# Kernel optimization log

Measured on AMD Instinct MI355X. Metric: run time of the kernel, lower is better.

Reference implementation:

```python
import jax, jax.numpy as jnp
import numpy as np

NUM_ENT = 10000
NUM_REL = 230
S_DIM = 96
T_DIM = 32
DIM = S_DIM + T_DIM  # 128
N = 32768   # neighbors
Q = 4096    # unique query entities
E = 32768   # pooling edges
B = 1024    # batch triples
BN_EPS = 1e-5


def setup_inputs() -> dict:
    key = jax.random.key(0)
    ks = jax.random.split(key, 32)
    inp = {}
    inp["neighbor_idx"] = jax.random.randint(ks[0], (N,), 0, NUM_ENT)
    inp["rel_id"] = jax.random.randint(ks[1], (N,), 0, 2 * NUM_REL)
    inp["years"] = jax.random.uniform(ks[2], (N, 1), jnp.float32)
    inp["months"] = jax.random.uniform(ks[3], (N, 1), jnp.float32)
    inp["days"] = jax.random.uniform(ks[4], (N, 1), jnp.float32)
    inp["pool_src"] = jax.random.randint(ks[5], (E,), 0, N)
    inp["pool_dst"] = jax.random.randint(ks[6], (E,), 0, Q)
    inp["head_pos"] = jax.random.randint(ks[7], (B,), 0, Q)
    inp["tail_pos"] = jax.random.randint(ks[8], (B,), 0, Q)
    inp["rels"] = jax.random.randint(ks[9], (B,), 0, NUM_REL)
    # parameters (xavier-ish scales)
    inp["ent_embs"] = jax.random.normal(ks[10], (NUM_ENT, S_DIM), jnp.float32) * 0.05
    names = ["y_freq", "y_phi", "y_amp", "m_freq", "m_phi", "m_amp", "d_freq", "d_phi", "d_amp"]
    for i, n in enumerate(names):
        inp[n] = jax.random.normal(ks[11 + i], (NUM_ENT, T_DIM), jnp.float32) * 0.05
    inp["rel_embs"] = jax.random.normal(ks[20], (NUM_REL, DIM), jnp.float32) * 0.05
    inp["W"] = jax.random.normal(ks[21], (2 * NUM_REL, DIM, DIM), jnp.float32) * (1.0 / np.sqrt(DIM))
    inp["b"] = jnp.zeros((2 * NUM_REL, DIM), jnp.float32)
    inp["gamma"] = jnp.ones((2 * NUM_REL, DIM), jnp.float32)
    inp["beta"] = jnp.zeros((2 * NUM_REL, DIM), jnp.float32)
    return inp


def _forward(ent_embs, y_freq, y_phi, y_amp, m_freq, m_phi, m_amp,
             d_freq, d_phi, d_amp, rel_embs, W, b, gamma, beta,
             years, months, days,
             neighbor_idx, rel_id, pool_src, pool_dst, head_pos, tail_pos, rels):
    # diachronic time embedding: amp * sin(freq * t + phi), summed over y/m/d
    ty = y_amp[neighbor_idx] * jnp.sin(y_freq[neighbor_idx] * years + y_phi[neighbor_idx])
    tm = m_amp[neighbor_idx] * jnp.sin(m_freq[neighbor_idx] * months + m_phi[neighbor_idx])
    td = d_amp[neighbor_idx] * jnp.sin(d_freq[neighbor_idx] * days + d_phi[neighbor_idx])
    x = jnp.concatenate([ent_embs[neighbor_idx], ty + tm + td], axis=1)  # [N, DIM]

    # per-relation Linear (gather weights per neighbor)
    z = jnp.einsum('nd,nde->ne', x, W[rel_id]) + b[rel_id]  # [N, DIM]

    # per-relation-bucket BatchNorm (training stats, biased var); skipped for singleton buckets
    R2 = 2 * NUM_REL
    cnt = jax.ops.segment_sum(jnp.ones((z.shape[0],), z.dtype), rel_id, num_segments=R2)
    denom = jnp.maximum(cnt, 1.0)[:, None]
    mean = jax.ops.segment_sum(z, rel_id, num_segments=R2) / denom
    var = jax.ops.segment_sum(z * z, rel_id, num_segments=R2) / denom - mean * mean
    var = jnp.maximum(var, 0.0)
    zn = (z - mean[rel_id]) * jax.lax.rsqrt(var[rel_id] + BN_EPS) * gamma[rel_id] + beta[rel_id]
    z = jnp.where((cnt[rel_id] > 1.0)[:, None], zn, z)
    z = jax.nn.relu(z)

    # average pooling of neighbor features per query entity (PoolingLayer 'avg')
    psum = jax.ops.segment_sum(z[pool_src], pool_dst, num_segments=Q)
    pcnt = jax.ops.segment_sum(jnp.ones((pool_src.shape[0],), z.dtype), pool_dst, num_segments=Q)
    emb = psum / jnp.maximum(pcnt, 1.0)[:, None]  # [Q, DIM]

    # TransE-style scoring: -||h + r - t||_2 (dropout p=0 / eval mode)
    diff = emb[head_pos] + rel_embs[rels] - emb[tail_pos]
    return -jnp.sqrt(jnp.sum(diff * diff, axis=1))


def reference(neighbor_idx, rel_id, years, months, days, pool_src, pool_dst,
              head_pos, tail_pos, rels, ent_embs, y_freq, y_phi, y_amp,
              m_freq, m_phi, m_amp, d_freq, d_phi, d_amp, rel_embs, W, b, gamma, beta):
    return _forward(ent_embs, y_freq, y_phi, y_amp, m_freq, m_phi, m_amp,
                    d_freq, d_phi, d_amp, rel_embs, W, b, gamma, beta,
                    years, months, days,
                    neighbor_idx, rel_id, pool_src, pool_dst, head_pos, tail_pos, rels)
```

## Files before the change

### kernel.cpp

```cpp
#include <hip/hip_runtime.h>
#include <math.h>

#define NUM_ENT 10000
#define NUM_REL 230
#define R2      460
#define S_DIM   96
#define T_DIM   32
#define DIM     128
#define N_NBR   32768
#define Q_ENT   4096
#define E_EDGE  32768
#define B_TRI   1024
#define BN_EPS  1e-5f
#define CHUNK   64

typedef __attribute__((ext_vector_type(8))) short bf16x8;
typedef __attribute__((ext_vector_type(4))) float f32x4;

__device__ __forceinline__ unsigned short f2bf(float f) {
    unsigned int u = __float_as_uint(f);
    u = (u + 0x7FFFu + ((u >> 16) & 1u)) >> 16;
    return (unsigned short)u;
}
__device__ __forceinline__ float bf2f(unsigned short us) {
    return __uint_as_float((unsigned int)us << 16);
}

__device__ __forceinline__ int XIDX(int m, int d) {
    return (m * DIM + d) ^ ((m & 7) << 3);
}

__global__ void k_zero(int* __restrict__ p, int n4) {
    int i = blockIdx.x * blockDim.x + threadIdx.x;
    if (i < n4) ((int4*)p)[i] = make_int4(0, 0, 0, 0);
}

__global__ __launch_bounds__(256, 2) void k_front(
    const float* __restrict__ W, unsigned short* __restrict__ Wfrag,
    const int* __restrict__ rel, const int* __restrict__ psrc,
    const int* __restrict__ pdst,
    int* __restrict__ hist_rel, int* __restrict__ histE,
    int* __restrict__ pcnt,
    int* __restrict__ ticket_n, int* __restrict__ ticket_e)
{
    const int t = threadIdx.x;
    if (blockIdx.x >= R2) {
        const int i = (blockIdx.x - R2) * 256 + t;
        if (i < N_NBR) ticket_n[i] = atomicAdd(&hist_rel[rel[i]], 1);
        if (i < E_EDGE) {
            const int s = psrc[i];
            ticket_e[i] = atomicAdd(&histE[rel[s]], 1);
            atomicAdd(&pcnt[pdst[i]], 1);
        }
        return;
    }
    const int r = blockIdx.x;
    __shared__ float Wl[DIM * DIM];
    {
        const float4* Wg = (const float4*)(W + (size_t)r * DIM * DIM);
        float4* Wl4 = (float4*)Wl;
        #pragma unroll
        for (int i = 0; i < 16; ++i)
            Wl4[t + i * 256] = Wg[t + i * 256];
    }
    __syncthreads();
    unsigned short* dst = Wfrag + (size_t)r * DIM * DIM;
    #pragma unroll
    for (int it = 0; it < 8; ++it) {
        const int id = t + it * 256;
        const int lane = id & 63;
        const int h    = (id >> 6) & 1;
        const int wv   = (id >> 7) & 3;
        const int kk   = (id >> 9) & 3;
        const int n  = 32 * wv + 16 * h + (lane & 15);
        const int kb = 32 * kk + 8 * (lane >> 4);
        ushort4 lo, hi;
        lo.x = f2bf(Wl[(kb + 0) * DIM + n]);
        lo.y = f2bf(Wl[(kb + 1) * DIM + n]);
        lo.z = f2bf(Wl[(kb + 2) * DIM + n]);
        lo.w = f2bf(Wl[(kb + 3) * DIM + n]);
        hi.x = f2bf(Wl[(kb + 4) * DIM + n]);
        hi.y = f2bf(Wl[(kb + 5) * DIM + n]);
        hi.z = f2bf(Wl[(kb + 6) * DIM + n]);
        hi.w = f2bf(Wl[(kb + 7) * DIM + n]);
        *(ushort4*)&dst[id * 8]     = lo;
        *(ushort4*)&dst[id * 8 + 4] = hi;
    }
}

__global__ __launch_bounds__(256) void k_place(
    const int* __restrict__ rel, const int* __restrict__ psrc,
    const int* __restrict__ pdst,
    const int* __restrict__ hist_rel, const int* __restrict__ histE,
    const int* __restrict__ ticket_n, const int* __restrict__ ticket_e,
    int* __restrict__ offsets, int* __restrict__ eoff,
    int* __restrict__ order, int* __restrict__ rankpack,
    int* __restrict__ epack)
{
    __shared__ int hA[512], hB[512], part[256];
    const int t = threadIdx.x;
    const int b = blockIdx.x;
    hA[t]       = (t < R2) ? hist_rel[t] : 0;
    hA[t + 256] = (t + 256 < R2) ? hist_rel[t + 256] : 0;
    hB[t]       = (t < R2) ? histE[t] : 0;
    hB[t + 256] = (t + 256 < R2) ? histE[t + 256] : 0;
    __syncthreads();

    const int a0 = hA[2 * t], a1 = hA[2 * t + 1];
    part[t] = a0 + a1;
    __syncthreads();
    for (int off = 1; off < 256; off <<= 1) {
        int v = (t >= off) ? part[t - off] : 0;
        __syncthreads();
        part[t] += v;
        __syncthreads();
    }
    {
        const int ex = t ? part[t - 1] : 0;
        hA[2 * t] = ex; hA[2 * t + 1] = ex + a0;
        if (b == 0) {
            if (2 * t < R2)     offsets[2 * t]     = ex;
            if (2 * t + 1 < R2) offsets[2 * t + 1] = ex + a0;
            if (t == 255)       offsets[R2]        = part[255];
        }
    }
    __syncthreads();

    const int b0 = hB[2 * t], b1 = hB[2 * t + 1];
    part[t] = b0 + b1;
    __syncthreads();
    for (int off = 1; off < 256; off <<= 1) {
        int v = (t >= off) ? part[t - off] : 0;
        __syncthreads();
        part[t] += v;
        __syncthreads();
    }
    {
        const int ex = t ? part[t - 1] : 0;
        hB[2 * t] = ex; hB[2 * t + 1] = ex + b0;
        if (b == 0) {
            if (2 * t < R2)     eoff[2 * t]     = ex;
            if (2 * t + 1 < R2) eoff[2 * t + 1] = ex + b0;
            if (t == 255)       eoff[R2]        = part[255];
        }
    }
    __syncthreads();

    const int i = b * 256 + t;
    if (i < N_NBR) {
        const int r = rel[i];
        const int pos = hA[r] + ticket_n[i];
        order[pos] = i;
        rankpack[i] = pos;
    }
    if (i < E_EDGE) {
        const int s = psrc[i];
        const int kr = rel[s];
        const int epos = hB[kr] + ticket_e[i];
        epack[epos] = s | (pdst[i] << 15);
    }
}

__global__ __launch_bounds__(512, 4) void k_matvec(
    const int* __restrict__ order, const int* __restrict__ offsets,
    const int* __restrict__ eoff, const int* __restrict__ epack,
    const int* __restrict__ rankpack,
    const int* __restrict__ nbr,
    const float* __restrict__ years, const float* __restrict__ months, const float* __restrict__ days,
    const float* __restrict__ ent,
    const float* __restrict__ yf, const float* __restrict__ yp, const float* __restrict__ ya,
    const float* __restrict__ mf, const float* __restrict__ mp, const float* __restrict__ ma,
    const float* __restrict__ df, const float* __restrict__ dp, const float* __restrict__ da,
    const unsigned short* __restrict__ Wfrag, const float* __restrict__ bias,
    const float* __restrict__ gamma, const float* __restrict__ beta,
    unsigned short* __restrict__ z_s, float* __restrict__ psum)
{
    const int r     = blockIdx.x;
    const int start = offsets[r];
    const int cnt   = offsets[r + 1] - start;

    __shared__ __align__(16) unsigned short Xl[2][CHUNK * DIM];
    __shared__ int s_ord[2][CHUNK];
    __shared__ int s_ni[2][CHUNK];
    __shared__ float bnred[8][2][16][2];
    __shared__ float scl[DIM], shf[DIM];

    const int t    = threadIdx.x;
    const int wid  = t >> 6;
    const int half = wid >> 2;
    const int wv   = wid & 3;
    const int lane = t & 63;
    const int l15  = lane & 15;
    const int g    = lane >> 4;

    const int nn0 = 32 * wv + l15;
    const int nn1 = nn0 + 16;
    const float bv0 = bias[r * DIM + nn0];
    const float bv1 = bias[r * DIM + nn1];

    float lsum0 = 0.f, lsq0 = 0.f, lsum1 = 0.f, lsq1 = 0.f;
    const unsigned short* Wr = Wfrag + (size_t)r * DIM * DIM;

    for (int cbase = 0; cbase < cnt; cbase += 2 * CHUNK) {
        const int hbase = cbase + half * CHUNK;
        const int mcnt  = min(CHUNK, max(0, cnt - hbase));

        if (t < 2 * CHUNK) {
            const int hh = t >> 6;
            const int m  = t & 63;
            const int gb = cbase + hh * CHUNK;
            int o = -1, ni = 0;
            if (gb + m < cnt) { o = order[start + gb + m]; ni = nbr[o]; }
            s_ord[hh][m] = o;
            s_ni[hh][m]  = ni;
        }
        __syncthreads();

        if (mcnt > 0) {
            const int lt = t & 255;
            const int m = lt >> 2, s = lt & 3;
            const int ni = s_ni[half][m];
            const bool vm = (m < mcnt);
            #pragma unroll
            for (int kk = 0; kk < 6; ++kk) {
                const int d = 4 * (s + 4 * kk);
                float4 e = *(const float4*)(ent + (size_t)ni * S_DIM + d);
                ushort4 b;
                b.x = vm ? f2bf(e.x) : 0; b.y = vm ? f2bf(e.y) : 0;
                b.z = vm ? f2bf(e.z) : 0; b.w = vm ? f2bf(e.w) : 0;
                *(ushort4*)&Xl[half][XIDX(m, d)] = b;
            }
            const int o = s_ord[half][m] < 0 ? 0 : s_ord[half][m];
            const float yr = years[o], mo = months[o], dy = days[o];
            #pragma unroll
            for (int hh = 0; hh < 2; ++hh) {
                const int j0 = s * 8 + hh * 4;
                const size_t tb = (size_t)ni * T_DIM + j0;
                const float4 vyf = *(const float4*)(yf + tb), vyp = *(const float4*)(yp + tb), vya = *(const float4*)(ya + tb);
                const float4 vmf = *(const float4*)(mf + tb), vmp = *(const float4*)(mp + tb), vma = *(const float4*)(ma + tb);
                const float4 vdf = *(const float4*)(df + tb), vdp = *(const float4*)(dp + tb), vda = *(const float4*)(da + tb);
                ushort4 b;
                #pragma unroll
                for (int j = 0; j < 4; ++j) {
                    const float fy = ((const float*)&vyf)[j] * yr + ((const float*)&vyp)[j];
                    const float fm = ((const float*)&vmf)[j] * mo + ((const float*)&vmp)[j];
                    const float fd = ((const float*)&vdf)[j] * dy + ((const float*)&vdp)[j];
                    float v = ((const float*)&vya)[j] * sinf(fy)
                            + ((const float*)&vma)[j] * sinf(fm)
                            + ((const float*)&vda)[j] * sinf(fd);
                    ((unsigned short*)&b)[j] = vm ? f2bf(v) : 0;
                }
                *(ushort4*)&Xl[half][XIDX(m, S_DIM + j0)] = b;
            }
        }
        __syncthreads();

        if (mcnt > 0) {
            f32x4 acc[4][2];
            #pragma unroll
            for (int i = 0; i < 4; ++i)
                #pragma unroll
                for (int j = 0; j < 2; ++j) acc[i][j] = (f32x4)0.f;

            #pragma unroll
            for (int kk = 0; kk < 4; ++kk) {
                const int k0 = kk * 32;
                bf16x8 a[4];
                #pragma unroll
                for (int mt = 0; mt < 4; ++mt)
                    a[mt] = *(const bf16x8*)&Xl[half][XIDX(16 * mt + l15, k0 + 8 * g)];
                const bf16x8 b0 = *(const bf16x8*)&Wr[(size_t)((kk * 4 + wv) * 2 + 0) * 512 + lane * 8];
                const bf16x8 b1 = *(const bf16x8*)&Wr[(size_t)((kk * 4 + wv) * 2 + 1) * 512 + lane * 8];
                #pragma unroll
                for (int mt = 0; mt < 4; ++mt) {
                    acc[mt][0] = __builtin_amdgcn_mfma_f32_16x16x32_bf16(a[mt], b0, acc[mt][0], 0, 0, 0);
                    acc[mt][1] = __builtin_amdgcn_mfma_f32_16x16x32_bf16(a[mt], b1, acc[mt][1], 0, 0, 0);
                }
            }

            #pragma unroll
            for (int mt = 0; mt < 4; ++mt) {
                #pragma unroll
                for (int reg = 0; reg < 4; ++reg) {
                    const int ml = 16 * mt + 4 * g + reg;
                    if (ml < mcnt) {
                        const float v0 = acc[mt][0][reg] + bv0;
                        const float v1 = acc[mt][1][reg] + bv1;
                        const size_t row = (size_t)(start + hbase + ml) * DIM;
                        z_s[row + nn0] = f2bf(v0);
                        z_s[row + nn1] = f2bf(v1);
                        lsum0 += v0; lsq0 += v0 * v0;
                        lsum1 += v1; lsq1 += v1 * v1;
                    }
                }
            }
        }
        __syncthreads();
    }

    lsum0 += __shfl_xor(lsum0, 16); lsum0 += __shfl_xor(lsum0, 32);
    lsq0  += __shfl_xor(lsq0, 16);  lsq0  += __shfl_xor(lsq0, 32);
    lsum1 += __shfl_xor(lsum1, 16); lsum1 += __shfl_xor(lsum1, 32);
    lsq1  += __shfl_xor(lsq1, 16);  lsq1  += __shfl_xor(lsq1, 32);
    if (g == 0) {
        bnred[wid][0][l15][0] = lsum0; bnred[wid][0][l15][1] = lsq0;
        bnred[wid][1][l15][0] = lsum1; bnred[wid][1][l15][1] = lsq1;
    }
    __syncthreads();
    if (half == 0 && g == 0) {
        #pragma unroll
        for (int nt = 0; nt < 2; ++nt) {
            const int col = 32 * wv + 16 * nt + l15;
            const float s = bnred[wid][nt][l15][0] + bnred[wid + 4][nt][l15][0];
            const float q = bnred[wid][nt][l15][1] + bnred[wid + 4][nt][l15][1];
            float sc = 1.f, sh = 0.f;
            if (cnt > 1) {
                const float mean = s / (float)cnt;
                const float var  = fmaxf(q / (float)cnt - mean * mean, 0.f);
                const int gi = r * DIM + col;
                sc = gamma[gi] * rsqrtf(var + BN_EPS);
                sh = beta[gi] - mean * sc;
            }
            scl[col] = sc;
            shf[col] = sh;
        }
    }
    __syncthreads();

    {
        const int e0 = eoff[r], e1 = eoff[r + 1];
        const int grp = t >> 7;
        const int d   = t & 127;
        const float psc = scl[d], psh = shf[d];
        for (int e = e0 + grp; e < e1; e += 4) {
            const int pk  = epack[e];
            const int s   = pk & 0x7FFF;
            const int q   = pk >> 15;
            const int row = rankpack[s];
            const float v = fmaxf(bf2f(z_s[(size_t)row * DIM + d]) * psc + psh, 0.f);
            atomicAdd(&psum[(size_t)q * DIM + d], v);
        }
    }
}

__global__ void k_score(const int* __restrict__ head, const int* __restrict__ tail,
                        const int* __restrict__ rels,
                        const float* __restrict__ psum, const int* __restrict__ pcnt,
                        const float* __restrict__ rel_embs,
                        float* __restrict__ out)
{
    const int b = blockIdx.x;
    const int d = threadIdx.x;
    const int h = head[b], tq = tail[b], r = rels[b];

    const float eh = psum[(size_t)h  * DIM + d] / fmaxf((float)pcnt[h],  1.f);
    const float et = psum[(size_t)tq * DIM + d] / fmaxf((float)pcnt[tq], 1.f);
    const float diff = eh + rel_embs[r * DIM + d] - et;
    float sq = diff * diff;
    for (int off = 32; off > 0; off >>= 1) sq += __shfl_down(sq, off);
    __shared__ float partial[2];
    if ((threadIdx.x & 63) == 0) partial[threadIdx.x >> 6] = sq;
    __syncthreads();
    if (threadIdx.x == 0) out[b] = -sqrtf(partial[0] + partial[1]);
}

extern "C" void kernel_launch(void* const* d_in, const int* in_sizes, int n_in,
                              void* d_out, int out_size, void* d_ws, size_t ws_size,
                              hipStream_t stream) {
    const int*   neighbor_idx = (const int*)  d_in[0];
    const int*   rel_id       = (const int*)  d_in[1];
    const float* years        = (const float*)d_in[2];
    const float* months       = (const float*)d_in[3];
    const float* days         = (const float*)d_in[4];
    const int*   pool_src     = (const int*)  d_in[5];
    const int*   pool_dst     = (const int*)  d_in[6];
    const int*   head_pos     = (const int*)  d_in[7];
    const int*   tail_pos     = (const int*)  d_in[8];
    const int*   rels         = (const int*)  d_in[9];
    const float* ent_embs     = (const float*)d_in[10];
    const float* y_freq       = (const float*)d_in[11];
    const float* y_phi        = (const float*)d_in[12];
    const float* y_amp        = (const float*)d_in[13];
    const float* m_freq       = (const float*)d_in[14];
    const float* m_phi        = (const float*)d_in[15];
    const float* m_amp        = (const float*)d_in[16];
    const float* d_freq       = (const float*)d_in[17];
    const float* d_phi        = (const float*)d_in[18];
    const float* d_amp        = (const float*)d_in[19];
    const float* rel_embs     = (const float*)d_in[20];
    const float* W            = (const float*)d_in[21];
    const float* bias         = (const float*)d_in[22];
    const float* gamma        = (const float*)d_in[23];
    const float* beta         = (const float*)d_in[24];

    float* out = (float*)d_out;

    float* ws = (float*)d_ws;
    size_t off = 0;
    unsigned short* Wfrag = (unsigned short*)(ws + off); off += (size_t)R2 * DIM * DIM / 2;
    unsigned short* z_s   = (unsigned short*)(ws + off); off += (size_t)N_NBR * DIM / 2;
    float* psum   = ws + off; off += (size_t)Q_ENT * DIM;
    int* pcnt     = (int*)(ws + off); off += Q_ENT;
    int* hist_rel = (int*)(ws + off); off += R2;
    int* histE    = (int*)(ws + off); off += R2;
    int* ticket_n = (int*)(ws + off); off += N_NBR;
    int* ticket_e = (int*)(ws + off); off += E_EDGE;
    int* offsets  = (int*)(ws + off); off += R2 + 1;
    int* eoff     = (int*)(ws + off); off += R2 + 1;
    int* order    = (int*)(ws + off); off += N_NBR;
    int* rankpack = (int*)(ws + off); off += N_NBR;
    int* epack    = (int*)(ws + off); off += E_EDGE;

    const int nzero  = Q_ENT * DIM + Q_ENT + 2 * R2;
    const int nzero4 = nzero / 4;
    k_zero<<<(nzero4 + 255) / 256, 256, 0, stream>>>((int*)psum, nzero4);

    k_front<<<R2 + (N_NBR + 255) / 256, 256, 0, stream>>>(
        W, Wfrag, rel_id, pool_src, pool_dst,
        hist_rel, histE, pcnt, ticket_n, ticket_e);

    k_place<<<(N_NBR + 255) / 256, 256, 0, stream>>>(
        rel_id, pool_src, pool_dst, hist_rel, histE,
        ticket_n, ticket_e, offsets, eoff, order, rankpack, epack);

    k_matvec<<<R2, 512, 0, stream>>>(order, offsets, eoff, epack, rankpack,
                                     neighbor_idx,
                                     years, months, days, ent_embs,
                                     y_freq, y_phi, y_amp,
                                     m_freq, m_phi, m_amp,
                                     d_freq, d_phi, d_amp,
                                     Wfrag, bias, gamma, beta,
                                     z_s, psum);

    k_score<<<B_TRI, DIM, 0, stream>>>(head_pos, tail_pos, rels,
                                       psum, pcnt, rel_embs, out);
}
```

Measured before the change: 79.55 us.

## Replace float atomic pooling with destination-sorted edge values reduced in scoring

Instead of atomically adding each pooled edge's activated feature into a per-query float accumulator, the edges are now bucketed by destination with a counting sort. Each edge's post-BN ReLU value is written as bf16 to its slot, and the scoring kernel sums only the slots belonging to each head and tail. This removes the large psum zeroing and the float atomics, and skips pooling for queries that are never scored. In exchange it adds a 4096-entry scan to every place block and a larger bf16 intermediate buffer, and it introduces bf16 rounding before summation.

```diff
diff --git a/kernel.cpp b/kernel.cpp
--- a/kernel.cpp
+++ b/kernel.cpp
@@ -40,8 +40,9 @@
     const int* __restrict__ rel, const int* __restrict__ psrc,
     const int* __restrict__ pdst,
     int* __restrict__ hist_rel, int* __restrict__ histE,
-    int* __restrict__ pcnt,
-    int* __restrict__ ticket_n, int* __restrict__ ticket_e)
+    int* __restrict__ hist_dst,
+    int* __restrict__ ticket_n, int* __restrict__ ticket_e,
+    int* __restrict__ ticket_d)
 {
     const int t = threadIdx.x;
     if (blockIdx.x >= R2) {
@@ -50,7 +51,7 @@
         if (i < E_EDGE) {
             const int s = psrc[i];
             ticket_e[i] = atomicAdd(&histE[rel[s]], 1);
-            atomicAdd(&pcnt[pdst[i]], 1);
+            ticket_d[i] = atomicAdd(&hist_dst[pdst[i]], 1);
         }
         return;
     }
@@ -92,18 +93,22 @@
     const int* __restrict__ rel, const int* __restrict__ psrc,
     const int* __restrict__ pdst,
     const int* __restrict__ hist_rel, const int* __restrict__ histE,
+    const int* __restrict__ hist_dst,
     const int* __restrict__ ticket_n, const int* __restrict__ ticket_e,
-    int* __restrict__ offsets, int* __restrict__ eoff,
-    int* __restrict__ order, int* __restrict__ rankpack,
-    int* __restrict__ epack)
+    const int* __restrict__ ticket_d,
+    int* __restrict__ offsets, int* __restrict__ eoff, int* __restrict__ dst_off,
+    int* __restrict__ order, int* __restrict__ epack)
 {
-    __shared__ int hA[512], hB[512], part[256];
+    __shared__ int hA[512], hE[512], hD[4096], part[256];
     const int t = threadIdx.x;
     const int b = blockIdx.x;
+
     hA[t]       = (t < R2) ? hist_rel[t] : 0;
     hA[t + 256] = (t + 256 < R2) ? hist_rel[t + 256] : 0;
-    hB[t]       = (t < R2) ? histE[t] : 0;
-    hB[t + 256] = (t + 256 < R2) ? histE[t + 256] : 0;
+    hE[t]       = (t < R2) ? histE[t] : 0;
+    hE[t + 256] = (t + 256 < R2) ? histE[t + 256] : 0;
+    #pragma unroll
+    for (int j = 0; j < 16; ++j) hD[t + j * 256] = hist_dst[t + j * 256];
     __syncthreads();
 
     const int a0 = hA[2 * t], a1 = hA[2 * t + 1];
@@ -126,7 +131,7 @@
     }
     __syncthreads();
 
-    const int b0 = hB[2 * t], b1 = hB[2 * t + 1];
+    const int b0 = hE[2 * t], b1 = hE[2 * t + 1];
     part[t] = b0 + b1;
     __syncthreads();
     for (int off = 1; off < 256; off <<= 1) {
@@ -137,7 +142,7 @@
     }
     {
         const int ex = t ? part[t - 1] : 0;
-        hB[2 * t] = ex; hB[2 * t + 1] = ex + b0;
+        hE[2 * t] = ex; hE[2 * t + 1] = ex + b0;
         if (b == 0) {
             if (2 * t < R2)     eoff[2 * t]     = ex;
             if (2 * t + 1 < R2) eoff[2 * t + 1] = ex + b0;
@@ -146,25 +151,46 @@
     }
     __syncthreads();
 
+    {
+        const int base = t * 16;
+        int v[16]; int lsum = 0;
+        #pragma unroll
+        for (int j = 0; j < 16; ++j) { v[j] = hD[base + j]; lsum += v[j]; }
+        part[t] = lsum;
+        __syncthreads();
+        for (int off = 1; off < 256; off <<= 1) {
+            int vv = (t >= off) ? part[t - off] : 0;
+            __syncthreads();
+            part[t] += vv;
+            __syncthreads();
+        }
+        int run = t ? part[t - 1] : 0;
+        #pragma unroll
+        for (int j = 0; j < 16; ++j) {
+            hD[base + j] = run;
+            if (b == 0) dst_off[base + j] = run;
+            run += v[j];
+        }
+        if (b == 0 && t == 255) dst_off[4096] = run;
+    }
+    __syncthreads();
+
     const int i = b * 256 + t;
     if (i < N_NBR) {
-        const int r = rel[i];
-        const int pos = hA[r] + ticket_n[i];
-        order[pos] = i;
-        rankpack[i] = pos;
+        order[hA[rel[i]] + ticket_n[i]] = i;
     }
     if (i < E_EDGE) {
         const int s = psrc[i];
-        const int kr = rel[s];
-        const int epos = hB[kr] + ticket_e[i];
-        epack[epos] = s | (pdst[i] << 15);
+        const int row  = hA[rel[s]] + ticket_n[s];
+        const int epos = hE[rel[s]] + ticket_e[i];
+        const int dpos = hD[pdst[i]] + ticket_d[i];
+        epack[epos] = row | (dpos << 15);
     }
 }
 
 __global__ __launch_bounds__(512, 4) void k_matvec(
     const int* __restrict__ order, const int* __restrict__ offsets,
     const int* __restrict__ eoff, const int* __restrict__ epack,
-    const int* __restrict__ rankpack,
     const int* __restrict__ nbr,
     const float* __restrict__ years, const float* __restrict__ months, const float* __restrict__ days,
     const float* __restrict__ ent,
@@ -173,7 +199,7 @@
     const float* __restrict__ df, const float* __restrict__ dp, const float* __restrict__ da,
     const unsigned short* __restrict__ Wfrag, const float* __restrict__ bias,
     const float* __restrict__ gamma, const float* __restrict__ beta,
-    unsigned short* __restrict__ z_s, float* __restrict__ psum)
+    unsigned short* __restrict__ z_s, unsigned short* __restrict__ eval)
 {
     const int r     = blockIdx.x;
     const int start = offsets[r];
@@ -333,19 +359,19 @@
         const int d   = t & 127;
         const float psc = scl[d], psh = shf[d];
         for (int e = e0 + grp; e < e1; e += 4) {
-            const int pk  = epack[e];
-            const int s   = pk & 0x7FFF;
-            const int q   = pk >> 15;
-            const int row = rankpack[s];
+            const int pk   = epack[e];
+            const int row  = pk & 0x7FFF;
+            const int dpos = pk >> 15;
             const float v = fmaxf(bf2f(z_s[(size_t)row * DIM + d]) * psc + psh, 0.f);
-            atomicAdd(&psum[(size_t)q * DIM + d], v);
+            eval[(size_t)dpos * DIM + d] = f2bf(v);
         }
     }
 }
 
 __global__ void k_score(const int* __restrict__ head, const int* __restrict__ tail,
                         const int* __restrict__ rels,
-                        const float* __restrict__ psum, const int* __restrict__ pcnt,
+                        const unsigned short* __restrict__ eval,
+                        const int* __restrict__ dst_off,
                         const float* __restrict__ rel_embs,
                         float* __restrict__ out)
 {
@@ -353,9 +379,18 @@
     const int d = threadIdx.x;
     const int h = head[b], tq = tail[b], r = rels[b];
 
-    const float eh = psum[(size_t)h  * DIM + d] / fmaxf((float)pcnt[h],  1.f);
-    const float et = psum[(size_t)tq * DIM + d] / fmaxf((float)pcnt[tq], 1.f);
-    const float diff = eh + rel_embs[r * DIM + d] - et;
+    const int h0 = dst_off[h],  h1 = dst_off[h + 1];
+    const int t0 = dst_off[tq], t1 = dst_off[tq + 1];
+
+    float fh = 0.f;
+    for (int e = h0; e < h1; ++e) fh += bf2f(eval[(size_t)e * DIM + d]);
+    fh /= (float)max(h1 - h0, 1);
+
+    float ft = 0.f;
+    for (int e = t0; e < t1; ++e) ft += bf2f(eval[(size_t)e * DIM + d]);
+    ft /= (float)max(t1 - t0, 1);
+
+    const float diff = fh + rel_embs[r * DIM + d] - ft;
     float sq = diff * diff;
     for (int off = 32; off > 0; off >>= 1) sq += __shfl_down(sq, off);
     __shared__ float partial[2];
@@ -399,39 +434,41 @@
     size_t off = 0;
     unsigned short* Wfrag = (unsigned short*)(ws + off); off += (size_t)R2 * DIM * DIM / 2;
     unsigned short* z_s   = (unsigned short*)(ws + off); off += (size_t)N_NBR * DIM / 2;
-    float* psum   = ws + off; off += (size_t)Q_ENT * DIM;
-    int* pcnt     = (int*)(ws + off); off += Q_ENT;
+    unsigned short* eval  = (unsigned short*)(ws + off); off += (size_t)E_EDGE * DIM / 2;
     int* hist_rel = (int*)(ws + off); off += R2;
     int* histE    = (int*)(ws + off); off += R2;
+    int* hist_dst = (int*)(ws + off); off += Q_ENT;
     int* ticket_n = (int*)(ws + off); off += N_NBR;
     int* ticket_e = (int*)(ws + off); off += E_EDGE;
+    int* ticket_d = (int*)(ws + off); off += E_EDGE;
     int* offsets  = (int*)(ws + off); off += R2 + 1;
     int* eoff     = (int*)(ws + off); off += R2 + 1;
+    int* dst_off  = (int*)(ws + off); off += Q_ENT + 1;
     int* order    = (int*)(ws + off); off += N_NBR;
-    int* rankpack = (int*)(ws + off); off += N_NBR;
     int* epack    = (int*)(ws + off); off += E_EDGE;
 
-    const int nzero  = Q_ENT * DIM + Q_ENT + 2 * R2;
-    const int nzero4 = nzero / 4;
-    k_zero<<<(nzero4 + 255) / 256, 256, 0, stream>>>((int*)psum, nzero4);
+    const int nzero  = 2 * R2 + Q_ENT;
+    const int nzero4 = (nzero + 3) / 4;
+    k_zero<<<(nzero4 + 255) / 256, 256, 0, stream>>>(hist_rel, nzero4);
 
     k_front<<<R2 + (N_NBR + 255) / 256, 256, 0, stream>>>(
         W, Wfrag, rel_id, pool_src, pool_dst,
-        hist_rel, histE, pcnt, ticket_n, ticket_e);
+        hist_rel, histE, hist_dst, ticket_n, ticket_e, ticket_d);
 
     k_place<<<(N_NBR + 255) / 256, 256, 0, stream>>>(
-        rel_id, pool_src, pool_dst, hist_rel, histE,
-        ticket_n, ticket_e, offsets, eoff, order, rankpack, epack);
-
-    k_matvec<<<R2, 512, 0, stream>>>(order, offsets, eoff, epack, rankpack,
+        rel_id, pool_src, pool_dst, hist_rel, histE, hist_dst,
+        ticket_n, ticket_e, ticket_d,
+        offsets, eoff, dst_off, order, epack);
+
+    k_matvec<<<R2, 512, 0, stream>>>(order, offsets, eoff, epack,
                                      neighbor_idx,
                                      years, months, days, ent_embs,
                                      y_freq, y_phi, y_amp,
                                      m_freq, m_phi, m_amp,
                                      d_freq, d_phi, d_amp,
                                      Wfrag, bias, gamma, beta,
-                                     z_s, psum);
+                                     z_s, eval);
 
     k_score<<<B_TRI, DIM, 0, stream>>>(head_pos, tail_pos, rels,
-                                       psum, pcnt, rel_embs, out);
-}
+                                       eval, dst_off, rel_embs, out);
+}
```

Result: faster. 74.81 us (-6.0%).
